# Optimization experiments

Measured on AMD Instinct MI355X. Metric: run time of the kernel, lower is better.

The kernel has to match this reference:

```python
import jax, jax.numpy as jnp
import numpy as np

_SHAPE = (4, 2, 8, 256, 513)  # N, 2(real/imag), C, T, F


def setup_inputs() -> dict:
    key = jax.random.key(0)
    k1, k2, k3 = jax.random.split(key, 3)
    return {
        "mixture": jax.random.normal(k1, _SHAPE, dtype=jnp.float32),
        "target": jax.random.normal(k2, _SHAPE, dtype=jnp.float32),
        "noise": jax.random.normal(k3, _SHAPE, dtype=jnp.float32),
        "ref_mic_idx": 0,
    }


def _to_complex(x):
    # (N, 2, C, T, F) real-imag stacked -> complex (N, C, T, F)
    return jax.lax.complex(x[:, 0], x[:, 1])


def _mean_spatial_cov(s):
    # s: complex (N, C, T, F) -> time-averaged covariance (N, F, C, C)
    N, C, T, F = s.shape
    sc = jnp.transpose(s, (0, 3, 2, 1))  # (N, F, T, C)
    # outer product V V^H summed over T, fused into one batched GEMM
    return jnp.einsum("nftc,nftd->nfcd", sc, jnp.conj(sc)) / T


def reference(mixture, target, noise, ref_mic_idx):
    y = _to_complex(mixture)  # (N, C, T, F)
    x = _to_complex(target)
    v = _to_complex(noise)
    N, C, T, F = y.shape

    phi_target = _mean_spatial_cov(x)  # (N, F, C, C)
    # diagonal loading: torch adds load to BOTH real and imag parts (RI dim broadcast)
    load = (0.001 / np.sqrt(2)) * (1.0 + 1.0j)
    phi_noise = _mean_spatial_cov(v) + jnp.asarray(load, dtype=y.dtype) * jnp.eye(C, dtype=y.dtype)

    G = jnp.linalg.inv(phi_noise) @ phi_target  # (N, F, C, C)
    l = jnp.trace(G, axis1=-2, axis2=-1)  # (N, F)
    # W = (1/l) * G @ e_ref  -> select column ref_mic_idx
    W = G[..., ref_mic_idx] / l[..., None]  # (N, F, C)

    # X_bf(n,t,f) = W^H y = sum_c conj(W)_{nfc} y_{nctf}
    X_bf = jnp.einsum("nfc,nctf->ntf", jnp.conj(W), y)  # (N, T, F)
    # restack real/imag and add singleton channel dim -> (N, 2, 1, T, F)
    out = jnp.stack([X_bf.real, X_bf.imag], axis=1)[:, :, None]
    return out
```

## Files before the change

kernel.cpp:

```cpp
#include <hip/hip_runtime.h>

#define Nn 4
#define Cc 8
#define Tt 256
#define Ff 513
#define TFs (Tt * Ff)
#define NPAIR 36

template <int G>
__device__ __forceinline__ void cov_body(const float* __restrict__ base,
                                         float* __restrict__ dst,
                                         int t0, int tchunk)
{
    constexpr int R2 = 7 - G;
    float ar[9], ai[9];
#pragma unroll
    for (int s = 0; s < 9; ++s) { ar[s] = 0.f; ai[s] = 0.f; }

    const float* bt = base + (size_t)t0 * Ff;
    for (int tt = 0; tt < tchunk; ++tt) {
        float re[8], im[8];
#pragma unroll
        for (int c = G; c < 8; ++c) {
            re[c] = bt[(size_t)c * TFs];
            im[c] = bt[(size_t)(Cc + c) * TFs];
        }
        int s = 0;
#pragma unroll
        for (int d = G; d < 8; ++d, ++s) {
            ar[s] += re[G] * re[d] + im[G] * im[d];
            ai[s] += im[G] * re[d] - re[G] * im[d];
        }
#pragma unroll
        for (int d = R2; d < 8; ++d, ++s) {
            ar[s] += re[R2] * re[d] + im[R2] * im[d];
            ai[s] += im[R2] * re[d] - re[R2] * im[d];
        }
        bt += Ff;
    }

    int s = 0;
#pragma unroll
    for (int d = G; d < 8; ++d, ++s) {
        const int p = G * 8 - G * (G - 1) / 2 + (d - G);
        dst[(size_t)(p * 2 + 0) * Ff] = ar[s];
        dst[(size_t)(p * 2 + 1) * Ff] = ai[s];
    }
#pragma unroll
    for (int d = R2; d < 8; ++d, ++s) {
        const int p = R2 * 8 - R2 * (R2 - 1) / 2 + (d - R2);
        dst[(size_t)(p * 2 + 0) * Ff] = ar[s];
        dst[(size_t)(p * 2 + 1) * Ff] = ai[s];
    }
}

__global__ __launch_bounds__(64) void cov_partial(
    const float* __restrict__ target, const float* __restrict__ noise,
    float* __restrict__ partial, int nchunk, int tchunk)
{
    int f = blockIdx.x * 64 + threadIdx.x;
    if (f >= Ff) return;
    int n = blockIdx.y;
    int z = blockIdx.z;
    int g = z & 3;
    int inp = (z >> 2) & 1;
    int chunk = z >> 3;

    const float* src = inp ? noise : target;
    const float* base = src + (size_t)n * 2 * Cc * TFs + f;
    float* dst = partial +
        ((((size_t)inp * Nn + n) * nchunk + chunk) * (NPAIR * 2)) * Ff + f;
    int t0 = chunk * tchunk;

    switch (g) {
        case 0: cov_body<0>(base, dst, t0, tchunk); break;
        case 1: cov_body<1>(base, dst, t0, tchunk); break;
        case 2: cov_body<2>(base, dst, t0, tchunk); break;
        default: cov_body<3>(base, dst, t0, tchunk); break;
    }
}

__global__ __launch_bounds__(64) void mvdr_weights(
    const float* __restrict__ partial, const int* __restrict__ ref_ptr,
    float2* __restrict__ wconj, int nchunk)
{
    const int lane = threadIdx.x;
    const int n = blockIdx.y;
    const int fbase = blockIdx.x * 4;

    __shared__ float cov[4][144];

    {
        int prob = lane & 3;
        int j = lane >> 2;
        int f = fbase + prob;
#pragma unroll
        for (int s = 0; s < 9; ++s) {
            int v = j * 9 + s;
            int inp = v >= 72;
            int p = inp ? v - 72 : v;
            float acc = 0.f;
            if (f < Ff) {
                for (int ch = 0; ch < nchunk; ++ch) {
                    size_t idx = ((((size_t)inp * Nn + n) * nchunk + ch) * 72 + p)
                                 * Ff + f;
                    acc += partial[idx];
                }
            }
            cov[prob][v] = acc;
        }
    }
    __syncthreads();

    const int prob = lane >> 4;
    const int col = lane & 15;
    const int f = fbase + prob;

    const float invT = 1.0f / (float)Tt;
    const float dl = 0.001f / 1.41421356237309515f;

    float Ar[8], Ai[8];
    {
        const bool left = (col < 8);
        const int c = left ? col : col - 8;
        const float* cv = &cov[prob][left ? 72 : 0];
#pragma unroll
        for (int r = 0; r < 8; ++r) {
            int lo = r <= c ? r : c, hi = r <= c ? c : r;
            int p = lo * 8 - lo * (lo - 1) / 2 + (hi - lo);
            float vr = cv[2 * p] * invT;
            float vi = cv[2 * p + 1] * invT;
            if (r > c) vi = -vi;
            if (left && r == c) { vr += dl; vi += dl; }
            Ar[r] = vr; Ai[r] = vi;
        }
    }

#pragma unroll
    for (int k = 0; k < 8; ++k) {
        int best = k;
        float bm = Ar[k] * Ar[k] + Ai[k] * Ai[k];
#pragma unroll
        for (int j = 0; j < 8; ++j) {
            if (j > k) {
                float m = Ar[j] * Ar[j] + Ai[j] * Ai[j];
                if (m > bm) { bm = m; best = j; }
            }
        }
        int bk = __shfl(best, k, 16);

        float tr = Ar[k], ti = Ai[k];
#pragma unroll
        for (int j = 0; j < 8; ++j) {
            if (j == bk && j != k) {
                Ar[k] = Ar[j]; Ai[k] = Ai[j];
                Ar[j] = tr;    Ai[j] = ti;
            }
        }

        float pr = __shfl(Ar[k], k, 16);
        float pi = __shfl(Ai[k], k, 16);
        float d = pr * pr + pi * pi;
        float ir = pr / d, ii = -pi / d;
        float nr = Ar[k] * ir - Ai[k] * ii;
        float ni = Ar[k] * ii + Ai[k] * ir;
        Ar[k] = nr; Ai[k] = ni;

#pragma unroll
        for (int r = 0; r < 8; ++r) {
            float fr = __shfl(Ar[r], k, 16);
            float fi = __shfl(Ai[r], k, 16);
            if (r != k) {
                Ar[r] -= fr * Ar[k] - fi * Ai[k];
                Ai[r] -= fr * Ai[k] + fi * Ar[k];
            }
        }
    }

    float tlr = 0.f, tli = 0.f;
    if (col >= 8) { tlr = Ar[col - 8]; tli = Ai[col - 8]; }
#pragma unroll
    for (int off = 1; off < 16; off <<= 1) {
        tlr += __shfl_xor(tlr, off, 16);
        tli += __shfl_xor(tli, off, 16);
    }

    int ref = *ref_ptr;
    if (col == 8 + ref && f < Ff) {
        float den = tlr * tlr + tli * tli;
        float2* wp = wconj + ((size_t)n * Ff + f) * 8;
#pragma unroll
        for (int r = 0; r < 8; ++r) {
            float wx = (Ar[r] * tlr + Ai[r] * tli) / den;
            float wy = (Ai[r] * tlr - Ar[r] * tli) / den;
            wp[r] = make_float2(wx, -wy);
        }
    }
}

__global__ __launch_bounds__(256) void beamform(
    const float* __restrict__ y, const float2* __restrict__ wconj,
    float* __restrict__ out)
{
    int idx = blockIdx.x * 256 + threadIdx.x;
    int n = idx / TFs;
    int rem = idx - n * TFs;
    int t = rem / Ff;
    int f = rem - t * Ff;

    size_t base_re = (size_t)n * 2 * Cc * TFs + (size_t)t * Ff + f;
    size_t base_im = base_re + (size_t)Cc * TFs;
    const float2* w = wconj + ((size_t)n * Ff + f) * 8;

    float xr = 0.f, xi = 0.f;
#pragma unroll
    for (int c = 0; c < Cc; ++c) {
        float yre = y[base_re + (size_t)c * TFs];
        float yim = y[base_im + (size_t)c * TFs];
        float2 wc = w[c];
        xr += wc.x * yre - wc.y * yim;
        xi += wc.x * yim + wc.y * yre;
    }
    size_t ob = (size_t)n * 2 * TFs + (size_t)t * Ff + f;
    out[ob] = xr;
    out[ob + TFs] = xi;
}

extern "C" void kernel_launch(void* const* d_in, const int* in_sizes, int n_in,
                              void* d_out, int out_size, void* d_ws, size_t ws_size,
                              hipStream_t stream) {
    const float* mixture = (const float*)d_in[0];
    const float* target  = (const float*)d_in[1];
    const float* noise   = (const float*)d_in[2];
    const int*   refp    = (const int*)d_in[3];
    float* out = (float*)d_out;

    const size_t wconj_bytes = (size_t)Nn * Ff * 8 * sizeof(float2);
    int nchunk = 8;
    while (nchunk > 1 &&
           (size_t)2 * Nn * nchunk * 72 * Ff * sizeof(float) + wconj_bytes > ws_size)
        nchunk >>= 1;
    int tchunk = Tt / nchunk;

    float*  partial = (float*)d_ws;
    float2* wconj = (float2*)((char*)d_ws +
                              (size_t)2 * Nn * nchunk * 72 * Ff * sizeof(float));

    cov_partial<<<dim3(9, Nn, nchunk * 8), 64, 0, stream>>>(
        target, noise, partial, nchunk, tchunk);
    mvdr_weights<<<dim3((Ff + 3) / 4, Nn), 64, 0, stream>>>(
        partial, refp, wconj, nchunk);
    beamform<<<dim3((Nn * TFs) / 256), 256, 0, stream>>>(mixture, wconj, out);
}
```

Measured before the change: 173.3 us.

## Merge covariance row groups per thread, batch MVDR solves, vectorize beamform

After: 200.7 us. +15.8%, slower.

```diff
diff --git a/kernel.cpp b/kernel.cpp
--- a/kernel.cpp
+++ b/kernel.cpp
@@ -7,64 +7,89 @@
 #define TFs (Tt * Ff)
 #define NPAIR 36
 
-template <int G>
-__device__ __forceinline__ void cov_body(const float* __restrict__ base,
-                                         float* __restrict__ dst,
-                                         int t0, int tchunk)
-{
-    constexpr int R2 = 7 - G;
-    float ar[9], ai[9];
-#pragma unroll
-    for (int s = 0; s < 9; ++s) { ar[s] = 0.f; ai[s] = 0.f; }
+template <int W>
+__device__ __forceinline__ void cov2_body(const float* __restrict__ base,
+                                          float* __restrict__ dst,
+                                          int t0, int tchunk)
+{
+    constexpr int G0 = 2 * W;
+    constexpr int G1 = 2 * W + 1;
+    constexpr int H0 = 7 - G0;
+    constexpr int H1 = 7 - G1;
+    float ar[18], ai[18];
+#pragma unroll
+    for (int s = 0; s < 18; ++s) { ar[s] = 0.f; ai[s] = 0.f; }
 
     const float* bt = base + (size_t)t0 * Ff;
     for (int tt = 0; tt < tchunk; ++tt) {
         float re[8], im[8];
 #pragma unroll
-        for (int c = G; c < 8; ++c) {
+        for (int c = G0; c < 8; ++c) {
             re[c] = bt[(size_t)c * TFs];
             im[c] = bt[(size_t)(Cc + c) * TFs];
         }
         int s = 0;
 #pragma unroll
-        for (int d = G; d < 8; ++d, ++s) {
-            ar[s] += re[G] * re[d] + im[G] * im[d];
-            ai[s] += im[G] * re[d] - re[G] * im[d];
-        }
-#pragma unroll
-        for (int d = R2; d < 8; ++d, ++s) {
-            ar[s] += re[R2] * re[d] + im[R2] * im[d];
-            ai[s] += im[R2] * re[d] - re[R2] * im[d];
+        for (int d = G0; d < 8; ++d, ++s) {
+            ar[s] += re[G0] * re[d] + im[G0] * im[d];
+            ai[s] += im[G0] * re[d] - re[G0] * im[d];
+        }
+#pragma unroll
+        for (int d = H0; d < 8; ++d, ++s) {
+            ar[s] += re[H0] * re[d] + im[H0] * im[d];
+            ai[s] += im[H0] * re[d] - re[H0] * im[d];
+        }
+#pragma unroll
+        for (int d = G1; d < 8; ++d, ++s) {
+            ar[s] += re[G1] * re[d] + im[G1] * im[d];
+            ai[s] += im[G1] * re[d] - re[G1] * im[d];
+        }
+#pragma unroll
+        for (int d = H1; d < 8; ++d, ++s) {
+            ar[s] += re[H1] * re[d] + im[H1] * im[d];
+            ai[s] += im[H1] * re[d] - re[H1] * im[d];
         }
         bt += Ff;
     }
 
     int s = 0;
 #pragma unroll
-    for (int d = G; d < 8; ++d, ++s) {
-        const int p = G * 8 - G * (G - 1) / 2 + (d - G);
-        dst[(size_t)(p * 2 + 0) * Ff] = ar[s];
-        dst[(size_t)(p * 2 + 1) * Ff] = ai[s];
-    }
-#pragma unroll
-    for (int d = R2; d < 8; ++d, ++s) {
-        const int p = R2 * 8 - R2 * (R2 - 1) / 2 + (d - R2);
-        dst[(size_t)(p * 2 + 0) * Ff] = ar[s];
-        dst[(size_t)(p * 2 + 1) * Ff] = ai[s];
-    }
-}
-
-__global__ __launch_bounds__(64) void cov_partial(
+    for (int d = G0; d < 8; ++d, ++s) {
+        const int p = G0 * 8 - G0 * (G0 - 1) / 2 + (d - G0);
+        dst[(size_t)(p * 2 + 0) * Ff] = ar[s];
+        dst[(size_t)(p * 2 + 1) * Ff] = ai[s];
+    }
+#pragma unroll
+    for (int d = H0; d < 8; ++d, ++s) {
+        const int p = H0 * 8 - H0 * (H0 - 1) / 2 + (d - H0);
+        dst[(size_t)(p * 2 + 0) * Ff] = ar[s];
+        dst[(size_t)(p * 2 + 1) * Ff] = ai[s];
+    }
+#pragma unroll
+    for (int d = G1; d < 8; ++d, ++s) {
+        const int p = G1 * 8 - G1 * (G1 - 1) / 2 + (d - G1);
+        dst[(size_t)(p * 2 + 0) * Ff] = ar[s];
+        dst[(size_t)(p * 2 + 1) * Ff] = ai[s];
+    }
+#pragma unroll
+    for (int d = H1; d < 8; ++d, ++s) {
+        const int p = H1 * 8 - H1 * (H1 - 1) / 2 + (d - H1);
+        dst[(size_t)(p * 2 + 0) * Ff] = ar[s];
+        dst[(size_t)(p * 2 + 1) * Ff] = ai[s];
+    }
+}
+
+__global__ __launch_bounds__(128) void cov_partial(
     const float* __restrict__ target, const float* __restrict__ noise,
     float* __restrict__ partial, int nchunk, int tchunk)
 {
-    int f = blockIdx.x * 64 + threadIdx.x;
+    int f = blockIdx.x * 64 + (threadIdx.x & 63);
     if (f >= Ff) return;
+    int w = threadIdx.x >> 6;
     int n = blockIdx.y;
     int z = blockIdx.z;
-    int g = z & 3;
-    int inp = (z >> 2) & 1;
-    int chunk = z >> 3;
+    int inp = z & 1;
+    int chunk = z >> 1;
 
     const float* src = inp ? noise : target;
     const float* base = src + (size_t)n * 2 * Cc * TFs + f;
@@ -72,48 +97,43 @@
         ((((size_t)inp * Nn + n) * nchunk + chunk) * (NPAIR * 2)) * Ff + f;
     int t0 = chunk * tchunk;
 
-    switch (g) {
-        case 0: cov_body<0>(base, dst, t0, tchunk); break;
-        case 1: cov_body<1>(base, dst, t0, tchunk); break;
-        case 2: cov_body<2>(base, dst, t0, tchunk); break;
-        default: cov_body<3>(base, dst, t0, tchunk); break;
-    }
-}
-
-__global__ __launch_bounds__(64) void mvdr_weights(
+    if (w == 0) cov2_body<0>(base, dst, t0, tchunk);
+    else        cov2_body<1>(base, dst, t0, tchunk);
+}
+
+__global__ __launch_bounds__(256) void mvdr_weights(
     const float* __restrict__ partial, const int* __restrict__ ref_ptr,
     float2* __restrict__ wconj, int nchunk)
 {
-    const int lane = threadIdx.x;
+    const int tid = threadIdx.x;
     const int n = blockIdx.y;
-    const int fbase = blockIdx.x * 4;
-
-    __shared__ float cov[4][144];
+    const int fbase = blockIdx.x * 16;
+
+    __shared__ float cov[16][144];
 
     {
-        int prob = lane & 3;
-        int j = lane >> 2;
-        int f = fbase + prob;
-#pragma unroll
-        for (int s = 0; s < 9; ++s) {
-            int v = j * 9 + s;
-            int inp = v >= 72;
+        int f_off = tid & 15;
+        int vrow = tid >> 4;
+        int f = fbase + f_off;
+#pragma unroll
+        for (int b = 0; b < 9; ++b) {
+            int v = b * 16 + vrow;
+            int inp = v >= 72 ? 1 : 0;
             int p = inp ? v - 72 : v;
             float acc = 0.f;
             if (f < Ff) {
-                for (int ch = 0; ch < nchunk; ++ch) {
-                    size_t idx = ((((size_t)inp * Nn + n) * nchunk + ch) * 72 + p)
-                                 * Ff + f;
-                    acc += partial[idx];
-                }
-            }
-            cov[prob][v] = acc;
+                const float* src = partial +
+                    (((size_t)inp * Nn + n) * nchunk * 72 + p) * Ff + f;
+                for (int ch = 0; ch < nchunk; ++ch)
+                    acc += src[(size_t)ch * 72 * Ff];
+            }
+            cov[f_off][v] = acc;
         }
     }
     __syncthreads();
 
-    const int prob = lane >> 4;
-    const int col = lane & 15;
+    const int prob = tid >> 4;
+    const int col = tid & 15;
     const int f = fbase + prob;
 
     const float invT = 1.0f / (float)Tt;
@@ -203,27 +223,29 @@
     float* __restrict__ out)
 {
     int idx = blockIdx.x * 256 + threadIdx.x;
-    int n = idx / TFs;
-    int rem = idx - n * TFs;
-    int t = rem / Ff;
-    int f = rem - t * Ff;
-
-    size_t base_re = (size_t)n * 2 * Cc * TFs + (size_t)t * Ff + f;
-    size_t base_im = base_re + (size_t)Cc * TFs;
-    const float2* w = wconj + ((size_t)n * Ff + f) * 8;
-
-    float xr = 0.f, xi = 0.f;
+    int n = idx / (TFs / 2);
+    int m = (idx - n * (TFs / 2)) * 2;
+    int f0 = m % Ff;
+    int f1 = (f0 + 1 == Ff) ? 0 : f0 + 1;
+
+    const float2* yb = (const float2*)y + ((size_t)n * 2 * Cc * TFs + m) / 2;
+    const float2* w0 = wconj + ((size_t)n * Ff + f0) * 8;
+    const float2* w1 = wconj + ((size_t)n * Ff + f1) * 8;
+
+    float xr0 = 0.f, xi0 = 0.f, xr1 = 0.f, xi1 = 0.f;
 #pragma unroll
     for (int c = 0; c < Cc; ++c) {
-        float yre = y[base_re + (size_t)c * TFs];
-        float yim = y[base_im + (size_t)c * TFs];
-        float2 wc = w[c];
-        xr += wc.x * yre - wc.y * yim;
-        xi += wc.x * yim + wc.y * yre;
-    }
-    size_t ob = (size_t)n * 2 * TFs + (size_t)t * Ff + f;
-    out[ob] = xr;
-    out[ob + TFs] = xi;
+        float2 yre = yb[(size_t)c * (TFs / 2)];
+        float2 yim = yb[(size_t)(Cc + c) * (TFs / 2)];
+        float2 a = w0[c], b = w1[c];
+        xr0 += a.x * yre.x - a.y * yim.x;
+        xi0 += a.x * yim.x + a.y * yre.x;
+        xr1 += b.x * yre.y - b.y * yim.y;
+        xi1 += b.x * yim.y + b.y * yre.y;
+    }
+    size_t ob = ((size_t)n * 2 * TFs + m) / 2;
+    ((float2*)out)[ob] = make_float2(xr0, xr1);
+    ((float2*)out)[ob + TFs / 2] = make_float2(xi0, xi1);
 }
 
 extern "C" void kernel_launch(void* const* d_in, const int* in_sizes, int n_in,
@@ -246,9 +268,9 @@
     float2* wconj = (float2*)((char*)d_ws +
                               (size_t)2 * Nn * nchunk * 72 * Ff * sizeof(float));
 
-    cov_partial<<<dim3(9, Nn, nchunk * 8), 64, 0, stream>>>(
+    cov_partial<<<dim3(9, Nn, nchunk * 2), 128, 0, stream>>>(
         target, noise, partial, nchunk, tchunk);
-    mvdr_weights<<<dim3((Ff + 3) / 4, Nn), 64, 0, stream>>>(
+    mvdr_weights<<<dim3((Ff + 15) / 16, Nn), 256, 0, stream>>>(
         partial, refp, wconj, nchunk);
-    beamform<<<dim3((Nn * TFs) / 256), 256, 0, stream>>>(mixture, wconj, out);
-}
+    beamform<<<dim3((Nn * TFs / 2) / 256), 256, 0, stream>>>(mixture, wconj, out);
+}
```
